# Optimization experiments

Measured on AMD Instinct MI355X. Metric: run time of the kernel, lower is better.

## Reference

```python
import jax, jax.numpy as jnp
import numpy as np

NB_CLASSES = 4
MRG = 0.05
ALPHA = 32.0
CL_W = 0.05
Z_PRUNE = 0.3
EPS = 1e-12


def _proxy_anchor(X, labels, valid, P):
    # X: [N, D] flattened span-pair features; labels: [N] int; valid: [N] float mask; P: [C, D]
    Xn = X / jnp.maximum(jnp.linalg.norm(X, axis=1, keepdims=True), EPS)
    Pn = P / jnp.maximum(jnp.linalg.norm(P, axis=1, keepdims=True), EPS)
    cos = Xn @ Pn.T  # [N, C]
    onehot = jax.nn.one_hot(labels, NB_CLASSES, dtype=cos.dtype)
    p_hot = onehot * valid[:, None]
    n_hot = (1.0 - onehot) * valid[:, None]
    pos_exp = jnp.exp(-ALPHA * (cos - MRG))
    neg_exp = jnp.exp(ALPHA * (cos + MRG))
    P_sim_sum = (p_hot * pos_exp).sum(axis=0)  # [C]
    N_sim_sum = (n_hot * neg_exp).sum(axis=0)  # [C]
    num_valid = jnp.maximum((p_hot.sum(axis=0) > 0).sum(), 1).astype(cos.dtype)
    pos_term = jnp.log1p(P_sim_sum).sum() / num_valid
    neg_term = jnp.log1p(N_sim_sum).sum() / NB_CLASSES
    return pos_term + neg_term


def _cl_loss(table, labels, attention_mask, P):
    B, L = table.shape[0], table.shape[1]
    lens = attention_mask.sum(axis=1)  # [B]
    idx = jnp.arange(L)
    rv = (idx[None, :] >= 1) & (idx[None, :] < (lens[:, None] - 1))  # [B, L]
    valid = (rv[:, :, None] & rv[:, None, :]).reshape(B, L * L).astype(table.dtype)
    X = table.reshape(B, L * L, -1)
    lab = labels.reshape(B, L * L)
    per_sample = jax.vmap(lambda x, l, v: _proxy_anchor(x, l, v, P))(X, lab, valid)
    return (CL_W * per_sample).mean()


def _span_pruning(pred, z, attention_mask):
    B = attention_mask.shape[0]
    mask_len = attention_mask.sum(axis=1) - 2
    length = (mask_len.astype(jnp.float32) * z).astype(jnp.int32)
    length = jnp.maximum(length, 10)
    length = jnp.minimum(length, mask_len * mask_len)
    pred_sort = -jnp.sort(-pred.reshape(B, -1), axis=1)  # descending
    topkth = pred_sort[jnp.arange(B), length - 1]
    return pred >= topkth[:, None, None]


def setup_inputs() -> dict:
    key = jax.random.key(0)
    ks = jax.random.split(key, 8)
    B, L, D = 4, 128, 768
    return {
        "table_edge": jax.random.normal(ks[0], (B, L, L, D), dtype=jnp.float32),
        "table_senti": jax.random.normal(ks[1], (B, L, L, D), dtype=jnp.float32),
        "attention_mask": jnp.ones((B, L), dtype=jnp.int32),
        "table_labels_S": jax.random.randint(ks[2], (B, L, L), 0, 2, dtype=jnp.int32),
        "table_labels_E": jax.random.randint(ks[3], (B, L, L), 0, 2, dtype=jnp.int32),
        "labels_edge": jax.random.randint(ks[4], (B, L, L), 0, 4, dtype=jnp.int32),
        "labels_senti": jax.random.randint(ks[5], (B, L, L), 0, 4, dtype=jnp.int32),
        "proxies_edge": jax.random.normal(ks[6], (4, D), dtype=jnp.float32),
        "proxies_senti": jax.random.normal(ks[7], (4, D), dtype=jnp.float32),
        "w_S": jax.random.normal(jax.random.fold_in(key, 10), (D,), dtype=jnp.float32) * 0.02,
        "b_S": jnp.zeros((1,), dtype=jnp.float32),
        "w_E": jax.random.normal(jax.random.fold_in(key, 11), (D,), dtype=jnp.float32) * 0.02,
        "b_E": jnp.zeros((1,), dtype=jnp.float32),
        "ID": 1,
        "epoch": 1,
    }


def reference(table_edge, table_senti, attention_mask, table_labels_S, table_labels_E,
              labels_edge, labels_senti, proxies_edge, proxies_senti,
              w_S, b_S, w_E, b_E, ID, epoch):
    cl_edge = _cl_loss(table_edge, labels_edge, attention_mask, proxies_edge)
    cl_senti = _cl_loss(table_senti, labels_senti, attention_mask, proxies_senti)

    logits_S = jnp.einsum('blmd,d->blm', table_edge, w_S) + b_S[0]
    logits_E = jnp.einsum('blmd,d->blm', table_edge, w_E) + b_E[0]

    weight = (table_labels_S >= 0).astype(logits_S.dtype)
    tS = table_labels_S.astype(logits_S.dtype)
    tE = table_labels_E.astype(logits_E.dtype)
    # BCEWithLogits: softplus(x) - x*t, weighted, mean over all elements
    loss_S = (weight * (jax.nn.softplus(logits_S) - logits_S * tS)).mean()
    loss_E = (weight * (jax.nn.softplus(logits_E) - logits_E * tE)).mean()

    S_pred = jax.nn.sigmoid(logits_S) * weight
    E_pred = jax.nn.sigmoid(logits_E) * weight
    pred_S = _span_pruning(S_pred, Z_PRUNE, attention_mask)
    pred_E = _span_pruning(E_pred, Z_PRUNE, attention_mask)

    return cl_edge, cl_senti, loss_S, loss_E, pred_S, pred_E
```

## Files before the change

### kernel.cpp

```cpp
#include <hip/hip_runtime.h>
#include <math.h>

#define LSEQ 128
#define NLL 16384
#define NBATCH 4
#define DIM 768
#define NB 4
#define ALPHA_C 32.0f
#define MRG_C 0.05f
#define CLW_C 0.05f
#define BPB 512
#define RSTR 72

__device__ __forceinline__ float wave_reduce_f(float v) {
#pragma unroll
    for (int s = 1; s < 64; s <<= 1) v += __shfl_xor(v, s);
    return v;
}

__device__ __forceinline__ float dot4(float4 a, float4 b) {
    return a.x*b.x + a.y*b.y + a.z*b.z + a.w*b.w;
}

template<bool EDGE>
__global__ __launch_bounds__(256, 2)
void fused_pass(const float* __restrict__ table,
                const int*   __restrict__ labels,
                const int*   __restrict__ attn,
                const float* __restrict__ prox,
                const float* __restrict__ wS, const float* __restrict__ bS,
                const float* __restrict__ wE, const float* __restrict__ bE,
                const int*   __restrict__ tlabS, const int* __restrict__ tlabE,
                float* __restrict__ pS, float* __restrict__ pE,
                float* __restrict__ partial )
{
    __shared__ float red[4][8*RSTR];
    __shared__ float sacc[4][14];

    const int tid = threadIdx.x, wib = tid >> 6, lane = tid & 63;
    const int g = blockIdx.x;
    const int b = g >> 9;
    const int wave_row0 = g*32 + wib*8;

    int lens_i = attn[b*LSEQ + lane] + attn[b*LSEQ + 64 + lane];
#pragma unroll
    for (int s = 1; s < 64; s <<= 1) lens_i += __shfl_xor(lens_i, s);

    const int lo4 = lane * 4;
    const float4 p00 = *(const float4*)(prox + 0*DIM +   0 + lo4);
    const float4 p01 = *(const float4*)(prox + 0*DIM + 256 + lo4);
    const float4 p02 = *(const float4*)(prox + 0*DIM + 512 + lo4);
    const float4 p10 = *(const float4*)(prox + 1*DIM +   0 + lo4);
    const float4 p11 = *(const float4*)(prox + 1*DIM + 256 + lo4);
    const float4 p12 = *(const float4*)(prox + 1*DIM + 512 + lo4);
    const float4 p20 = *(const float4*)(prox + 2*DIM +   0 + lo4);
    const float4 p21 = *(const float4*)(prox + 2*DIM + 256 + lo4);
    const float4 p22 = *(const float4*)(prox + 2*DIM + 512 + lo4);
    const float4 p30 = *(const float4*)(prox + 3*DIM +   0 + lo4);
    const float4 p31 = *(const float4*)(prox + 3*DIM + 256 + lo4);
    const float4 p32 = *(const float4*)(prox + 3*DIM + 512 + lo4);
    float pinv0, pinv1, pinv2, pinv3;
    {
        float s0 = dot4(p00,p00)+dot4(p01,p01)+dot4(p02,p02);
        float s1 = dot4(p10,p10)+dot4(p11,p11)+dot4(p12,p12);
        float s2 = dot4(p20,p20)+dot4(p21,p21)+dot4(p22,p22);
        float s3 = dot4(p30,p30)+dot4(p31,p31)+dot4(p32,p32);
        s0 = wave_reduce_f(s0); s1 = wave_reduce_f(s1);
        s2 = wave_reduce_f(s2); s3 = wave_reduce_f(s3);
        pinv0 = 1.0f / fmaxf(sqrtf(s0), 1e-12f);
        pinv1 = 1.0f / fmaxf(sqrtf(s1), 1e-12f);
        pinv2 = 1.0f / fmaxf(sqrtf(s2), 1e-12f);
        pinv3 = 1.0f / fmaxf(sqrtf(s3), 1e-12f);
    }
    float4 vs0, vs1, vs2, ve0, ve1, ve2;
    if constexpr (EDGE) {
        vs0 = *(const float4*)(wS +   0 + lo4);
        vs1 = *(const float4*)(wS + 256 + lo4);
        vs2 = *(const float4*)(wS + 512 + lo4);
        ve0 = *(const float4*)(wE +   0 + lo4);
        ve1 = *(const float4*)(wE + 256 + lo4);
        ve2 = *(const float4*)(wE + 512 + lo4);
    }

    const float* rowp = table + (size_t)wave_row0 * DIM + lo4;
    float* rw = red[wib];

#pragma unroll 1
    for (int rr = 0; rr < 8; ++rr) {
        const float* xb = rowp + rr*DIM;
        const float4 x0 = *(const float4*)(xb);
        const float4 x1 = *(const float4*)(xb + 256);
        const float4 x2 = *(const float4*)(xb + 512);
        float xx = dot4(x0,x0) + dot4(x1,x1) + dot4(x2,x2);
        float d0 = dot4(x0,p00) + dot4(x1,p01) + dot4(x2,p02);
        float d1 = dot4(x0,p10) + dot4(x1,p11) + dot4(x2,p12);
        float d2 = dot4(x0,p20) + dot4(x1,p21) + dot4(x2,p22);
        float d3 = dot4(x0,p30) + dot4(x1,p31) + dot4(x2,p32);
        float dS, dE;
        if constexpr (EDGE) {
            dS = dot4(x0,vs0) + dot4(x1,vs1) + dot4(x2,vs2);
            dE = dot4(x0,ve0) + dot4(x1,ve1) + dot4(x2,ve2);
        }
#pragma unroll
        for (int s = 1; s < 8; s <<= 1) {
            xx += __shfl_xor(xx, s);
            d0 += __shfl_xor(d0, s); d1 += __shfl_xor(d1, s);
            d2 += __shfl_xor(d2, s); d3 += __shfl_xor(d3, s);
            if constexpr (EDGE) { dS += __shfl_xor(dS, s); dE += __shfl_xor(dE, s); }
        }
        if ((lane & 7) == 0) {
            float* dst = rw + rr*RSTR + (lane >> 3) * 8;
            *(float4*)dst = make_float4(xx, d0, d1, d2);
            if constexpr (EDGE) {
                *(float2*)(dst + 4) = make_float2(d3, dS);
                dst[6] = dE;
            } else {
                dst[4] = d3;
            }
        }
    }

    const int v = lane >> 3, myr = lane & 7;
    float S = 0.f;
    constexpr int NV = EDGE ? 7 : 5;
    if (v < NV) {
#pragma unroll
        for (int gz = 0; gz < 8; ++gz) S += rw[myr*RSTR + gz*8 + v];
    }
    const float gxx = __shfl(S, 0*8 + myr);
    const float gd0 = __shfl(S, 1*8 + myr);
    const float gd1 = __shfl(S, 2*8 + myr);
    const float gd2 = __shfl(S, 3*8 + myr);
    const float gd3 = __shfl(S, 4*8 + myr);
    float gdS = 0.f, gdE = 0.f;
    if constexpr (EDGE) {
        gdS = __shfl(S, 5*8 + myr);
        gdE = __shfl(S, 6*8 + myr);
    }

    float Pa0=0,Pa1=0,Pa2=0,Pa3=0, Na0=0,Na1=0,Na2=0,Na3=0, Ca0=0,Ca1=0,Ca2=0,Ca3=0;
    float sBS = 0.f, sBE = 0.f;
    if (lane < 8) {
        const int r = wave_row0 + myr;
        const int i = r & (NLL - 1);
        const int l = i >> 7, m = i & (LSEQ - 1);
        const bool valid = (l >= 1) && (l < lens_i - 1) && (m >= 1) && (m < lens_i - 1);
        if (valid) {
            const int lab = labels[r];
            const float xinv = 1.0f / fmaxf(sqrtf(gxx), 1e-12f);
            const float c0 = gd0 * xinv * pinv0;
            const float c1 = gd1 * xinv * pinv1;
            const float c2 = gd2 * xinv * pinv2;
            const float c3 = gd3 * xinv * pinv3;
            if (lab == 0) { Pa0 = expf(-ALPHA_C*(c0 - MRG_C)); Ca0 = 1.f; }
            else          { Na0 = expf( ALPHA_C*(c0 + MRG_C)); }
            if (lab == 1) { Pa1 = expf(-ALPHA_C*(c1 - MRG_C)); Ca1 = 1.f; }
            else          { Na1 = expf( ALPHA_C*(c1 + MRG_C)); }
            if (lab == 2) { Pa2 = expf(-ALPHA_C*(c2 - MRG_C)); Ca2 = 1.f; }
            else          { Na2 = expf( ALPHA_C*(c2 + MRG_C)); }
            if (lab == 3) { Pa3 = expf(-ALPHA_C*(c3 - MRG_C)); Ca3 = 1.f; }
            else          { Na3 = expf( ALPHA_C*(c3 + MRG_C)); }
        }
        if constexpr (EDGE) {
            const float xSl = gdS + bS[0], xEl = gdE + bE[0];
            const int ls = tlabS[r], le = tlabE[r];
            const float w = (ls >= 0) ? 1.f : 0.f;
            const float spS = fmaxf(xSl, 0.f) + log1pf(expf(-fabsf(xSl)));
            const float spE = fmaxf(xEl, 0.f) + log1pf(expf(-fabsf(xEl)));
            sBS = w * (spS - xSl * (float)ls);
            sBE = w * (spE - xEl * (float)le);
            pS[r] = w / (1.f + expf(-xSl));
            pE[r] = w / (1.f + expf(-xEl));
        }
    }
#pragma unroll
    for (int s = 1; s < 8; s <<= 1) {
        Pa0 += __shfl_xor(Pa0, s); Pa1 += __shfl_xor(Pa1, s);
        Pa2 += __shfl_xor(Pa2, s); Pa3 += __shfl_xor(Pa3, s);
        Na0 += __shfl_xor(Na0, s); Na1 += __shfl_xor(Na1, s);
        Na2 += __shfl_xor(Na2, s); Na3 += __shfl_xor(Na3, s);
        Ca0 += __shfl_xor(Ca0, s); Ca1 += __shfl_xor(Ca1, s);
        Ca2 += __shfl_xor(Ca2, s); Ca3 += __shfl_xor(Ca3, s);
        sBS += __shfl_xor(sBS, s); sBE += __shfl_xor(sBE, s);
    }
    if (lane == 0) {
        float* sp = sacc[wib];
        sp[0]=Pa0; sp[1]=Pa1; sp[2]=Pa2; sp[3]=Pa3;
        sp[4]=Na0; sp[5]=Na1; sp[6]=Na2; sp[7]=Na3;
        sp[8]=Ca0; sp[9]=Ca1; sp[10]=Ca2; sp[11]=Ca3;
        sp[12]=sBS; sp[13]=sBE;
    }
    __syncthreads();
    if (tid < 14) {
        const float s = sacc[0][tid] + sacc[1][tid] + sacc[2][tid] + sacc[3][tid];
        const int blk = g & (BPB - 1);
        partial[(b * 14 + tid) * BPB + blk] = s;
    }
}

__global__ __launch_bounds__(1024)
void tail_k(const float* __restrict__ pS, const float* __restrict__ pE,
            const int* __restrict__ attn,
            const float* __restrict__ partE, const float* __restrict__ partS,
            float* __restrict__ out)
{
    __shared__ unsigned sh[NLL];
    __shared__ int csum[16];
    __shared__ float gg[56];
    const int tid = threadIdx.x, wave = tid >> 6, lane = tid & 63;

    if (blockIdx.x >= 8) {
        const int tbl = blockIdx.x - 8;
        const float* part = (tbl == 0) ? partE : partS;
        for (int grp = wave; grp < 56; grp += 16) {
            float s = 0.f;
#pragma unroll
            for (int j = lane; j < BPB; j += 64) s += part[grp*BPB + j];
            s = wave_reduce_f(s);
            if (lane == 0) gg[grp] = s;
        }
        __syncthreads();
        if (tid == 0) {
            float tot = 0.f;
            for (int b = 0; b < NBATCH; ++b) {
                const float* G = gg + b * 14;
                int nv = 0;
                for (int c = 0; c < NB; ++c) nv += (G[8+c] > 0.f) ? 1 : 0;
                const float nvf = (float)((nv > 1) ? nv : 1);
                float pos = 0.f, neg = 0.f;
                for (int c = 0; c < NB; ++c) { pos += log1pf(G[c]); neg += log1pf(G[4+c]); }
                tot += pos / nvf + neg * 0.25f;
            }
            out[tbl] = CLW_C * tot * 0.25f;
            if (tbl == 0) {
                float bs = 0.f, be = 0.f;
                for (int b = 0; b < NBATCH; ++b) { bs += gg[b*14 + 12]; be += gg[b*14 + 13]; }
                out[2] = bs * (1.0f / 65536.0f);
                out[3] = be * (1.0f / 65536.0f);
            }
        }
        return;
    }

    const int a = blockIdx.x >> 2;
    const int b = blockIdx.x & 3;
    const float* p = (a ? pE : pS) + (size_t)b * NLL;
    float* o = out + 4 + (size_t)a * (NBATCH * NLL) + (size_t)b * NLL;

    int asum = attn[b*LSEQ + lane] + attn[b*LSEQ + 64 + lane];
#pragma unroll
    for (int s = 1; s < 64; s <<= 1) asum += __shfl_xor(asum, s);
    const int mask_len = asum - 2;
    int k = (int)((float)mask_len * 0.3f);
    k = (k > 10) ? k : 10;
    const int ml2 = mask_len * mask_len;
    k = (k < ml2) ? k : ml2;

    for (int j = tid; j < NLL; j += 1024) sh[j] = __float_as_uint(p[j]);
    __syncthreads();

    unsigned lo = 0u, hi = 0x3F800000u;
    for (int it = 0; it < 32; ++it) {
        if (lo >= hi) break;
        const unsigned span = hi - lo;
        const unsigned mid = lo + (span >> 1) + (span & 1u);
        int c = 0;
        for (int j = tid; j < NLL; j += 1024) c += (sh[j] >= mid) ? 1 : 0;
#pragma unroll
        for (int s = 1; s < 64; s <<= 1) c += __shfl_xor(c, s);
        if (lane == 0) csum[wave] = c;
        __syncthreads();
        int tot = 0;
#pragma unroll
        for (int w = 0; w < 16; ++w) tot += csum[w];
        if (tot >= k) lo = mid; else hi = mid - 1u;
        __syncthreads();
    }

    for (int j = tid; j < NLL; j += 1024) o[j] = (sh[j] >= lo) ? 1.0f : 0.0f;
}

extern "C" void kernel_launch(void* const* d_in, const int* in_sizes, int n_in,
                              void* d_out, int out_size, void* d_ws, size_t ws_size,
                              hipStream_t stream)
{
    const float* table_edge  = (const float*)d_in[0];
    const float* table_senti = (const float*)d_in[1];
    const int*   attn        = (const int*)d_in[2];
    const int*   tlabS       = (const int*)d_in[3];
    const int*   tlabE       = (const int*)d_in[4];
    const int*   lab_edge    = (const int*)d_in[5];
    const int*   lab_senti   = (const int*)d_in[6];
    const float* prox_edge   = (const float*)d_in[7];
    const float* prox_senti  = (const float*)d_in[8];
    const float* w_S         = (const float*)d_in[9];
    const float* b_S         = (const float*)d_in[10];
    const float* w_E         = (const float*)d_in[11];
    const float* b_E         = (const float*)d_in[12];

    float* out   = (float*)d_out;
    float* ws    = (float*)d_ws;
    float* pS    = ws;
    float* pE    = ws + 65536;
    float* partE = ws + 131072;
    float* partS = partE + 28672;

    fused_pass<true><<<2048, 256, 0, stream>>>(table_edge, lab_edge, attn, prox_edge,
        w_S, b_S, w_E, b_E, tlabS, tlabE, pS, pE, partE);
    fused_pass<false><<<2048, 256, 0, stream>>>(table_senti, lab_senti, attn, prox_senti,
        nullptr, nullptr, nullptr, nullptr, nullptr, nullptr, nullptr, nullptr, partS);
    tail_k<<<10, 1024, 0, stream>>>(pS, pE, attn, partE, partS, out);
}
```

Before: 128.1 us.

## Merge edge and senti passes into one launch with row prefetch

Combines the two per-table fused_pass launches into a single 4096-block kernel in which blocks alternate between the edge and senti tables. The 8-row loop is fully unrolled and software-pipelined, loading the next row's float4 values while computing the current row's dot products. Launch bounds go from 2 to 4 blocks per CU. Together these aim to remove one launch gap and keep more memory traffic in flight on this bandwidth-bound read of two 200MB tables, at the cost of more registers per thread, which the tighter occupancy target may force into spills.

```diff
diff --git a/kernel.cpp b/kernel.cpp
--- a/kernel.cpp
+++ b/kernel.cpp
@@ -23,22 +23,16 @@
 }
 
 template<bool EDGE>
-__global__ __launch_bounds__(256, 2)
-void fused_pass(const float* __restrict__ table,
-                const int*   __restrict__ labels,
-                const int*   __restrict__ attn,
-                const float* __restrict__ prox,
-                const float* __restrict__ wS, const float* __restrict__ bS,
-                const float* __restrict__ wE, const float* __restrict__ bE,
-                const int*   __restrict__ tlabS, const int* __restrict__ tlabE,
-                float* __restrict__ pS, float* __restrict__ pE,
-                float* __restrict__ partial )
+__device__ __forceinline__ void pass_body(
+    const float* __restrict__ table, const int* __restrict__ labels,
+    const int* __restrict__ attn, const float* __restrict__ prox,
+    const float* __restrict__ wS, const float* __restrict__ bS,
+    const float* __restrict__ wE, const float* __restrict__ bE,
+    const int* __restrict__ tlabS, const int* __restrict__ tlabE,
+    float* __restrict__ pS, float* __restrict__ pE,
+    float* __restrict__ partial, float* __restrict__ rw, float* __restrict__ sacc_all,
+    int g, int wib, int lane, int tid)
 {
-    __shared__ float red[4][8*RSTR];
-    __shared__ float sacc[4][14];
-
-    const int tid = threadIdx.x, wib = tid >> 6, lane = tid & 63;
-    const int g = blockIdx.x;
     const int b = g >> 9;
     const int wave_row0 = g*32 + wib*8;
 
@@ -83,23 +77,28 @@
     }
 
     const float* rowp = table + (size_t)wave_row0 * DIM + lo4;
-    float* rw = red[wib];
-
-#pragma unroll 1
+
+    float4 a0 = *(const float4*)(rowp);
+    float4 a1 = *(const float4*)(rowp + 256);
+    float4 a2 = *(const float4*)(rowp + 512);
+#pragma unroll
     for (int rr = 0; rr < 8; ++rr) {
-        const float* xb = rowp + rr*DIM;
-        const float4 x0 = *(const float4*)(xb);
-        const float4 x1 = *(const float4*)(xb + 256);
-        const float4 x2 = *(const float4*)(xb + 512);
-        float xx = dot4(x0,x0) + dot4(x1,x1) + dot4(x2,x2);
-        float d0 = dot4(x0,p00) + dot4(x1,p01) + dot4(x2,p02);
-        float d1 = dot4(x0,p10) + dot4(x1,p11) + dot4(x2,p12);
-        float d2 = dot4(x0,p20) + dot4(x1,p21) + dot4(x2,p22);
-        float d3 = dot4(x0,p30) + dot4(x1,p31) + dot4(x2,p32);
+        float4 n0, n1, n2;
+        if (rr < 7) {
+            const float* nx = rowp + (rr+1)*DIM;
+            n0 = *(const float4*)(nx);
+            n1 = *(const float4*)(nx + 256);
+            n2 = *(const float4*)(nx + 512);
+        }
+        float xx = dot4(a0,a0) + dot4(a1,a1) + dot4(a2,a2);
+        float d0 = dot4(a0,p00) + dot4(a1,p01) + dot4(a2,p02);
+        float d1 = dot4(a0,p10) + dot4(a1,p11) + dot4(a2,p12);
+        float d2 = dot4(a0,p20) + dot4(a1,p21) + dot4(a2,p22);
+        float d3 = dot4(a0,p30) + dot4(a1,p31) + dot4(a2,p32);
         float dS, dE;
         if constexpr (EDGE) {
-            dS = dot4(x0,vs0) + dot4(x1,vs1) + dot4(x2,vs2);
-            dE = dot4(x0,ve0) + dot4(x1,ve1) + dot4(x2,ve2);
+            dS = dot4(a0,vs0) + dot4(a1,vs1) + dot4(a2,vs2);
+            dE = dot4(a0,ve0) + dot4(a1,ve1) + dot4(a2,ve2);
         }
 #pragma unroll
         for (int s = 1; s < 8; s <<= 1) {
@@ -118,6 +117,7 @@
                 dst[4] = d3;
             }
         }
+        a0 = n0; a1 = n1; a2 = n2;
     }
 
     const int v = lane >> 3, myr = lane & 7;
@@ -184,7 +184,7 @@
         sBS += __shfl_xor(sBS, s); sBE += __shfl_xor(sBE, s);
     }
     if (lane == 0) {
-        float* sp = sacc[wib];
+        float* sp = sacc_all + wib*14;
         sp[0]=Pa0; sp[1]=Pa1; sp[2]=Pa2; sp[3]=Pa3;
         sp[4]=Na0; sp[5]=Na1; sp[6]=Na2; sp[7]=Na3;
         sp[8]=Ca0; sp[9]=Ca1; sp[10]=Ca2; sp[11]=Ca3;
@@ -192,10 +192,36 @@
     }
     __syncthreads();
     if (tid < 14) {
-        const float s = sacc[0][tid] + sacc[1][tid] + sacc[2][tid] + sacc[3][tid];
+        const float s = sacc_all[0*14+tid] + sacc_all[1*14+tid]
+                      + sacc_all[2*14+tid] + sacc_all[3*14+tid];
         const int blk = g & (BPB - 1);
         partial[(b * 14 + tid) * BPB + blk] = s;
     }
+}
+
+__global__ __launch_bounds__(256, 4)
+void fused_pass(const float* __restrict__ tabE, const float* __restrict__ tabS,
+                const int* __restrict__ labE, const int* __restrict__ labSen,
+                const int* __restrict__ attn,
+                const float* __restrict__ proxE, const float* __restrict__ proxSen,
+                const float* __restrict__ wS, const float* __restrict__ bS,
+                const float* __restrict__ wE, const float* __restrict__ bE,
+                const int* __restrict__ tlabS, const int* __restrict__ tlabE,
+                float* __restrict__ pS, float* __restrict__ pE,
+                float* __restrict__ partE, float* __restrict__ partSen)
+{
+    __shared__ float red[4][8*RSTR];
+    __shared__ float sacc[4*14];
+    const int tid = threadIdx.x, wib = tid >> 6, lane = tid & 63;
+    const int tbl = blockIdx.x & 1;
+    const int g = blockIdx.x >> 1;
+    if (tbl == 0)
+        pass_body<true >(tabE, labE, attn, proxE, wS, bS, wE, bE, tlabS, tlabE,
+                         pS, pE, partE, red[wib], sacc, g, wib, lane, tid);
+    else
+        pass_body<false>(tabS, labSen, attn, proxSen, nullptr, nullptr, nullptr, nullptr,
+                         nullptr, nullptr, nullptr, nullptr, partSen, red[wib], sacc,
+                         g, wib, lane, tid);
 }
 
 __global__ __launch_bounds__(1024)
@@ -305,9 +331,8 @@
     float* partE = ws + 131072;
     float* partS = partE + 28672;
 
-    fused_pass<true><<<2048, 256, 0, stream>>>(table_edge, lab_edge, attn, prox_edge,
-        w_S, b_S, w_E, b_E, tlabS, tlabE, pS, pE, partE);
-    fused_pass<false><<<2048, 256, 0, stream>>>(table_senti, lab_senti, attn, prox_senti,
-        nullptr, nullptr, nullptr, nullptr, nullptr, nullptr, nullptr, nullptr, partS);
+    fused_pass<<<4096, 256, 0, stream>>>(table_edge, table_senti,
+        lab_edge, lab_senti, attn, prox_edge, prox_senti,
+        w_S, b_S, w_E, b_E, tlabS, tlabE, pS, pE, partE, partS);
     tail_k<<<10, 1024, 0, stream>>>(pS, pE, attn, partE, partS, out);
 }
```

Result: slower. 135.7 us (+6.0%).

## Merge edge and senti passes into one launch with LDS weights and full-wave shuffles

Applied to the files above, without the earlier changes.

Replaces the two per-table kernel launches with a single 4096-block launch, where even blocks process the edge table and odd blocks the senti table. The classifier weights move from registers into LDS, read through volatile loads, to cut register pressure. The LDS-based cross-group reduction is replaced by full 64-lane shuffle reductions per row, with each row's result kept by the matching lane. This removes one launch and the tail of the first kernel, at the cost of more shuffle instructions per row, volatile LDS reads on every row, and dropping the min-2-blocks launch bound.

```diff
diff --git a/kernel.cpp b/kernel.cpp
--- a/kernel.cpp
+++ b/kernel.cpp
@@ -10,7 +10,6 @@
 #define MRG_C 0.05f
 #define CLW_C 0.05f
 #define BPB 512
-#define RSTR 72
 
 __device__ __forceinline__ float wave_reduce_f(float v) {
 #pragma unroll
@@ -22,23 +21,21 @@
     return a.x*b.x + a.y*b.y + a.z*b.z + a.w*b.w;
 }
 
+__device__ __forceinline__ float4 ldsv4(const float* p) {
+    const volatile float* q = p;
+    return make_float4(q[0], q[1], q[2], q[3]);
+}
+
 template<bool EDGE>
-__global__ __launch_bounds__(256, 2)
-void fused_pass(const float* __restrict__ table,
-                const int*   __restrict__ labels,
-                const int*   __restrict__ attn,
-                const float* __restrict__ prox,
-                const float* __restrict__ wS, const float* __restrict__ bS,
-                const float* __restrict__ wE, const float* __restrict__ bE,
-                const int*   __restrict__ tlabS, const int* __restrict__ tlabE,
-                float* __restrict__ pS, float* __restrict__ pE,
-                float* __restrict__ partial )
+__device__ __forceinline__ void pass_body(
+    const float* __restrict__ table, const int* __restrict__ labels,
+    const int* __restrict__ attn, const float* __restrict__ prox,
+    const float* __restrict__ bS, const float* __restrict__ bE,
+    const int* __restrict__ tlabS, const int* __restrict__ tlabE,
+    float* __restrict__ pS, float* __restrict__ pE,
+    float* __restrict__ partial, const float* __restrict__ wlds,
+    float* __restrict__ sacc_all, int g, int wib, int lane, int tid)
 {
-    __shared__ float red[4][8*RSTR];
-    __shared__ float sacc[4][14];
-
-    const int tid = threadIdx.x, wib = tid >> 6, lane = tid & 63;
-    const int g = blockIdx.x;
     const int b = g >> 9;
     const int wave_row0 = g*32 + wib*8;
 
@@ -72,18 +69,10 @@
         pinv2 = 1.0f / fmaxf(sqrtf(s2), 1e-12f);
         pinv3 = 1.0f / fmaxf(sqrtf(s3), 1e-12f);
     }
-    float4 vs0, vs1, vs2, ve0, ve1, ve2;
-    if constexpr (EDGE) {
-        vs0 = *(const float4*)(wS +   0 + lo4);
-        vs1 = *(const float4*)(wS + 256 + lo4);
-        vs2 = *(const float4*)(wS + 512 + lo4);
-        ve0 = *(const float4*)(wE +   0 + lo4);
-        ve1 = *(const float4*)(wE + 256 + lo4);
-        ve2 = *(const float4*)(wE + 512 + lo4);
-    }
 
     const float* rowp = table + (size_t)wave_row0 * DIM + lo4;
-    float* rw = red[wib];
+
+    float s_xx=0, s_d0=0, s_d1=0, s_d2=0, s_d3=0, s_dS=0, s_dE=0;
 
 #pragma unroll 1
     for (int rr = 0; rr < 8; ++rr) {
@@ -98,60 +87,40 @@
         float d3 = dot4(x0,p30) + dot4(x1,p31) + dot4(x2,p32);
         float dS, dE;
         if constexpr (EDGE) {
-            dS = dot4(x0,vs0) + dot4(x1,vs1) + dot4(x2,vs2);
-            dE = dot4(x0,ve0) + dot4(x1,ve1) + dot4(x2,ve2);
-        }
-#pragma unroll
-        for (int s = 1; s < 8; s <<= 1) {
+            dS = dot4(x0, ldsv4(wlds +   0 + lo4))
+               + dot4(x1, ldsv4(wlds + 256 + lo4))
+               + dot4(x2, ldsv4(wlds + 512 + lo4));
+            dE = dot4(x0, ldsv4(wlds + DIM +   0 + lo4))
+               + dot4(x1, ldsv4(wlds + DIM + 256 + lo4))
+               + dot4(x2, ldsv4(wlds + DIM + 512 + lo4));
+        }
+#pragma unroll
+        for (int s = 1; s < 64; s <<= 1) {
             xx += __shfl_xor(xx, s);
             d0 += __shfl_xor(d0, s); d1 += __shfl_xor(d1, s);
             d2 += __shfl_xor(d2, s); d3 += __shfl_xor(d3, s);
             if constexpr (EDGE) { dS += __shfl_xor(dS, s); dE += __shfl_xor(dE, s); }
         }
-        if ((lane & 7) == 0) {
-            float* dst = rw + rr*RSTR + (lane >> 3) * 8;
-            *(float4*)dst = make_float4(xx, d0, d1, d2);
-            if constexpr (EDGE) {
-                *(float2*)(dst + 4) = make_float2(d3, dS);
-                dst[6] = dE;
-            } else {
-                dst[4] = d3;
-            }
-        }
-    }
-
-    const int v = lane >> 3, myr = lane & 7;
-    float S = 0.f;
-    constexpr int NV = EDGE ? 7 : 5;
-    if (v < NV) {
-#pragma unroll
-        for (int gz = 0; gz < 8; ++gz) S += rw[myr*RSTR + gz*8 + v];
-    }
-    const float gxx = __shfl(S, 0*8 + myr);
-    const float gd0 = __shfl(S, 1*8 + myr);
-    const float gd1 = __shfl(S, 2*8 + myr);
-    const float gd2 = __shfl(S, 3*8 + myr);
-    const float gd3 = __shfl(S, 4*8 + myr);
-    float gdS = 0.f, gdE = 0.f;
-    if constexpr (EDGE) {
-        gdS = __shfl(S, 5*8 + myr);
-        gdE = __shfl(S, 6*8 + myr);
+        if (lane == rr) {
+            s_xx = xx; s_d0 = d0; s_d1 = d1; s_d2 = d2; s_d3 = d3;
+            if constexpr (EDGE) { s_dS = dS; s_dE = dE; }
+        }
     }
 
     float Pa0=0,Pa1=0,Pa2=0,Pa3=0, Na0=0,Na1=0,Na2=0,Na3=0, Ca0=0,Ca1=0,Ca2=0,Ca3=0;
     float sBS = 0.f, sBE = 0.f;
     if (lane < 8) {
-        const int r = wave_row0 + myr;
+        const int r = wave_row0 + lane;
         const int i = r & (NLL - 1);
         const int l = i >> 7, m = i & (LSEQ - 1);
         const bool valid = (l >= 1) && (l < lens_i - 1) && (m >= 1) && (m < lens_i - 1);
         if (valid) {
             const int lab = labels[r];
-            const float xinv = 1.0f / fmaxf(sqrtf(gxx), 1e-12f);
-            const float c0 = gd0 * xinv * pinv0;
-            const float c1 = gd1 * xinv * pinv1;
-            const float c2 = gd2 * xinv * pinv2;
-            const float c3 = gd3 * xinv * pinv3;
+            const float xinv = 1.0f / fmaxf(sqrtf(s_xx), 1e-12f);
+            const float c0 = s_d0 * xinv * pinv0;
+            const float c1 = s_d1 * xinv * pinv1;
+            const float c2 = s_d2 * xinv * pinv2;
+            const float c3 = s_d3 * xinv * pinv3;
             if (lab == 0) { Pa0 = expf(-ALPHA_C*(c0 - MRG_C)); Ca0 = 1.f; }
             else          { Na0 = expf( ALPHA_C*(c0 + MRG_C)); }
             if (lab == 1) { Pa1 = expf(-ALPHA_C*(c1 - MRG_C)); Ca1 = 1.f; }
@@ -162,7 +131,7 @@
             else          { Na3 = expf( ALPHA_C*(c3 + MRG_C)); }
         }
         if constexpr (EDGE) {
-            const float xSl = gdS + bS[0], xEl = gdE + bE[0];
+            const float xSl = s_dS + bS[0], xEl = s_dE + bE[0];
             const int ls = tlabS[r], le = tlabE[r];
             const float w = (ls >= 0) ? 1.f : 0.f;
             const float spS = fmaxf(xSl, 0.f) + log1pf(expf(-fabsf(xSl)));
@@ -184,7 +153,7 @@
         sBS += __shfl_xor(sBS, s); sBE += __shfl_xor(sBE, s);
     }
     if (lane == 0) {
-        float* sp = sacc[wib];
+        float* sp = sacc_all + wib*14;
         sp[0]=Pa0; sp[1]=Pa1; sp[2]=Pa2; sp[3]=Pa3;
         sp[4]=Na0; sp[5]=Na1; sp[6]=Na2; sp[7]=Na3;
         sp[8]=Ca0; sp[9]=Ca1; sp[10]=Ca2; sp[11]=Ca3;
@@ -192,9 +161,42 @@
     }
     __syncthreads();
     if (tid < 14) {
-        const float s = sacc[0][tid] + sacc[1][tid] + sacc[2][tid] + sacc[3][tid];
+        const float s = sacc_all[0*14+tid] + sacc_all[1*14+tid]
+                      + sacc_all[2*14+tid] + sacc_all[3*14+tid];
         const int blk = g & (BPB - 1);
         partial[(b * 14 + tid) * BPB + blk] = s;
+    }
+}
+
+__global__ __launch_bounds__(256)
+void fused_pass(const float* __restrict__ tabE, const float* __restrict__ tabS,
+                const int* __restrict__ labE, const int* __restrict__ labSen,
+                const int* __restrict__ attn,
+                const float* __restrict__ proxE, const float* __restrict__ proxSen,
+                const float* __restrict__ wS, const float* __restrict__ bS,
+                const float* __restrict__ wE, const float* __restrict__ bE,
+                const int* __restrict__ tlabS, const int* __restrict__ tlabE,
+                float* __restrict__ pS, float* __restrict__ pE,
+                float* __restrict__ partE, float* __restrict__ partSen)
+{
+    __shared__ float wlds[2*DIM];
+    __shared__ float sacc[4*14];
+    const int tid = threadIdx.x, wib = tid >> 6, lane = tid & 63;
+    const int tbl = blockIdx.x & 1;
+    const int g = blockIdx.x >> 1;
+    if (tbl == 0) {
+        for (int i = tid; i < 384; i += 256) {
+            const float* src = (i < 192) ? (wS + i*4) : (wE + (i-192)*4);
+            *reinterpret_cast<float4*>(&wlds[i*4]) = *reinterpret_cast<const float4*>(src);
+        }
+        __syncthreads();
+        pass_body<true >(tabE, labE, attn, proxE, bS, bE, tlabS, tlabE,
+                         pS, pE, partE, wlds, sacc, g, wib, lane, tid);
+    } else {
+        __syncthreads();
+        pass_body<false>(tabS, labSen, attn, proxSen, nullptr, nullptr,
+                         nullptr, nullptr, nullptr, nullptr, partSen, wlds, sacc,
+                         g, wib, lane, tid);
     }
 }
 
@@ -305,9 +307,8 @@
     float* partE = ws + 131072;
     float* partS = partE + 28672;
 
-    fused_pass<true><<<2048, 256, 0, stream>>>(table_edge, lab_edge, attn, prox_edge,
-        w_S, b_S, w_E, b_E, tlabS, tlabE, pS, pE, partE);
-    fused_pass<false><<<2048, 256, 0, stream>>>(table_senti, lab_senti, attn, prox_senti,
-        nullptr, nullptr, nullptr, nullptr, nullptr, nullptr, nullptr, nullptr, partS);
+    fused_pass<<<4096, 256, 0, stream>>>(table_edge, table_senti,
+        lab_edge, lab_senti, attn, prox_edge, prox_senti,
+        w_S, b_S, w_E, b_E, tlabS, tlabE, pS, pE, partE, partS);
     tail_k<<<10, 1024, 0, stream>>>(pS, pE, attn, partE, partS, out);
 }
```

Result: slower. 164.0 us (+28.0%).
